# Performance work log

Hardware: AMD Instinct MI355X
Metric: run time of the kernel (lower is better)

## Reference

```python
import jax, jax.numpy as jnp
import numpy as np

B, S, DM, H, HD = 2, 2048, 1024, 16, 64
MEM_SIZE = 1000
K_SIMILAR, K_CONTIG = 8, 2
K_TOTAL = K_SIMILAR + K_CONTIG  # 10 memory tokens
NEG = -1e9


def setup_inputs() -> dict:
    key = jax.random.key(0)
    k1, k2, k3, k4, k5, k6 = jax.random.split(key, 6)
    inputs = jax.random.normal(k1, (B, S, DM), dtype=jnp.float32)
    attention_mask = jnp.ones((B, S), dtype=jnp.float32)
    Wq = jax.random.normal(k2, (DM, H * HD), dtype=jnp.float32) * 0.02
    Wk = jax.random.normal(k3, (DM, H * HD), dtype=jnp.float32) * 0.02
    Wv = jax.random.normal(k4, (DM, H * HD), dtype=jnp.float32) * 0.02
    Wo = jax.random.normal(k5, (H * HD, DM), dtype=jnp.float32) * 0.02
    events = jax.random.normal(k6, (MEM_SIZE, H * HD), dtype=jnp.float32) * 0.02
    return {"inputs": inputs, "attention_mask": attention_mask,
            "Wq": Wq, "Wk": Wk, "Wv": Wv, "Wo": Wo, "events": events}


def _forward(inputs, attention_mask, Wq, Wk, Wv, Wo, events):
    # projections (no bias), split heads: [B, H, S, HD]
    q = (inputs @ Wq).reshape(B, S, H, HD).transpose(0, 2, 1, 3)
    k = (inputs @ Wk).reshape(B, S, H, HD).transpose(0, 2, 1, 3)
    v = (inputs @ Wv).reshape(B, S, H, HD).transpose(0, 2, 1, 3)

    # --- episodic retrieval: cosine top-k of last-token key vs events ---
    qvec = k[:, :, -1, :].reshape(B, H * HD)                       # [B, D]
    qn = qvec / (jnp.linalg.norm(qvec, axis=-1, keepdims=True) + 1e-8)
    en = events / (jnp.linalg.norm(events, axis=-1, keepdims=True) + 1e-8)
    sims = qn @ en.T                                               # [B, M]
    _, topk_idx = jax.lax.top_k(sims, K_TOTAL)                     # [B, K]
    retrieved = events[topk_idx]                                   # [B, K, D]
    retrieved_k = retrieved.reshape(B, K_TOTAL, H, HD).transpose(0, 2, 1, 3)  # [B,H,K,HD]
    retrieved_v = retrieved_k                                      # non-differential path

    aug_k = jnp.concatenate([retrieved_k, k], axis=2)              # [B,H,K+S,HD]
    aug_v = jnp.concatenate([retrieved_v, v], axis=2)

    # --- ALiBi bias: slopes * (pos_i - pos_j) on original cols, 0 on memory cols ---
    slopes = 2.0 ** (-8.0 * jnp.arange(1, H + 1, dtype=jnp.float32) / H)  # [H]
    positions = jnp.arange(S, dtype=jnp.float32)
    pos_diff = positions[:, None] - positions[None, :]             # [S, S]
    alibi = slopes[:, None, None] * pos_diff                       # [H, S, S]
    alibi = jnp.concatenate([jnp.zeros((H, S, K_TOTAL), jnp.float32), alibi], axis=-1)

    # --- causal mask: -1e9 strictly-upper on original cols, 0 on memory cols ---
    tri = jnp.where(jnp.arange(S)[None, :] > jnp.arange(S)[:, None], NEG, 0.0)  # [S,S]
    causal = jnp.concatenate([jnp.zeros((S, K_TOTAL), jnp.float32), tri], axis=-1)

    # --- padding mask: memory tokens always attendable ---
    aug_mask = jnp.concatenate([jnp.ones((B, K_TOTAL), jnp.float32), attention_mask], axis=-1)
    mask_bias = (1.0 - aug_mask)[:, None, None, :] * NEG           # [B,1,1,K+S]

    scores = jnp.einsum("bhqd,bhkd->bhqk", q, aug_k) / np.sqrt(HD)
    scores = scores + alibi[None] + causal[None, None] + mask_bias
    attn = jax.nn.softmax(scores, axis=-1)
    out = jnp.einsum("bhqk,bhkd->bhqd", attn, aug_v)               # [B,H,S,HD]
    out = out.transpose(0, 2, 1, 3).reshape(B, S, H * HD)
    return out @ Wo


def reference(inputs, attention_mask, Wq, Wk, Wv, Wo, events):
    return _forward(inputs, attention_mask, Wq, Wk, Wv, Wo, events)
```

## Files before the change

kernel.cpp:

```cpp
#include <hip/hip_runtime.h>
#include <hip/hip_bf16.h>
#include <math.h>

#define B_   2
#define S_   2048
#define DM_  1024
#define H_   16
#define HD_  64
#define MEM_ 1000
#define KTOT 10
#define NROW (B_ * S_)
#define NEG9 (-1e9f)
#define LDK  72

#define NUNITS  1440
#define NSPLITI 416
#define PSLOT   4224
#define SC_  0.18033688f
#define TH_  170.238f

typedef __attribute__((ext_vector_type(8))) short short8;
typedef __attribute__((ext_vector_type(4))) float f32x4;

__device__ __forceinline__ float __exp2(float x) { return __builtin_amdgcn_exp2f(x); }

__device__ __forceinline__ void gll16(const __hip_bfloat16* g, __hip_bfloat16* l) {
    __builtin_amdgcn_global_load_lds(
        (const __attribute__((address_space(1))) void*)g,
        (__attribute__((address_space(3))) void*)l, 16, 0, 0);
}

__global__ __launch_bounds__(256) void prep(const float* __restrict__ inputs,
                                            const float* __restrict__ Wq,
                                            const float* __restrict__ Wk,
                                            const float* __restrict__ Wv,
                                            const float* __restrict__ Wo,
                                            __hip_bfloat16* __restrict__ Ax,
                                            __hip_bfloat16* __restrict__ Wt,
                                            float* __restrict__ lk,
                                            int* __restrict__ ctr) {
    const int bx = blockIdx.x, tid = threadIdx.x;
    if (bx == 0 && tid == 0) *ctr = 0;

    if (bx < 2048) {
        const size_t i = ((size_t)bx * 256 + tid) * 8;
        float4 a = *(const float4*)&inputs[i];
        float4 b = *(const float4*)&inputs[i + 4];
        alignas(16) __hip_bfloat16 t[8];
        t[0] = __float2bfloat16(a.x); t[1] = __float2bfloat16(a.y);
        t[2] = __float2bfloat16(a.z); t[3] = __float2bfloat16(a.w);
        t[4] = __float2bfloat16(b.x); t[5] = __float2bfloat16(b.y);
        t[6] = __float2bfloat16(b.z); t[7] = __float2bfloat16(b.w);
        *(short8*)&Ax[i] = *(short8*)t;
        return;
    }
    if (bx < 3072) {
        const int idx = bx - 2048;
        const int g = idx >> 8, rem = idx & 255;
        const float* W = (g == 0) ? Wq : (g == 1) ? Wk : (g == 2) ? Wv : Wo;
        const int n0 = (rem & 15) * 64, k0 = (rem >> 4) * 64;
        __shared__ float T[64][65];
        {
            const int r = tid >> 4, c4 = (tid & 15) * 4;
#pragma unroll
            for (int p = 0; p < 4; ++p) {
                float4 v = *(const float4*)&W[(size_t)(k0 + r + p * 16) * 1024 + n0 + c4];
                T[r + p * 16][c4 + 0] = v.x; T[r + p * 16][c4 + 1] = v.y;
                T[r + p * 16][c4 + 2] = v.z; T[r + p * 16][c4 + 3] = v.w;
            }
        }
        __syncthreads();
        {
            const int n = tid >> 3, off = (tid & 7) * 8;
#pragma unroll
            for (int p = 0; p < 2; ++p) {
                const int nn = n + p * 32;
                alignas(16) __hip_bfloat16 t[8];
#pragma unroll
                for (int j = 0; j < 8; ++j) t[j] = __float2bfloat16(T[off + j][nn]);
                *(short8*)&Wt[((size_t)(g * 1024 + n0 + nn)) * 1024 + k0 + off] = *(short8*)t;
            }
        }
        return;
    }
    {
        const int idx = bx - 3072;
        const int xblk = idx & 15, b = idx >> 4;
        const int cl = tid & 63;
        const int col = xblk * 64 + cl;
        const int kq = tid >> 6;
        __shared__ float xr[1024];
        __shared__ float part[4][64];
        for (int i = tid; i < 1024; i += 256)
            xr[i] = inputs[((size_t)(b * S_ + S_ - 1)) * 1024 + i];
        __syncthreads();
        float acc = 0.f;
#pragma unroll 4
        for (int k = kq * 256; k < kq * 256 + 256; ++k)
            acc += xr[k] * Wk[(size_t)k * 1024 + col];
        part[kq][cl] = acc;
        __syncthreads();
        if (tid < 64)
            lk[b * 1024 + xblk * 64 + tid] =
                part[0][tid] + part[1][tid] + part[2][tid] + part[3][tid];
    }
}

__device__ __forceinline__ void store_out(__hip_bfloat16* p, float x) { *p = __float2bfloat16(x); }
__device__ __forceinline__ void store_out(float* p, float x) { *p = x; }

template <typename OutT>
__global__ __launch_bounds__(256) void gemm_mfma(const __hip_bfloat16* __restrict__ A,
                                                 const __hip_bfloat16* __restrict__ Bt,
                                                 OutT* __restrict__ C, int ldc) {
    __shared__ __hip_bfloat16 As[128 * 32];
    __shared__ __hip_bfloat16 Bs[128 * 32];
    const int tid = threadIdx.x;
    const int wave = tid >> 6, lane = tid & 63;
    const int quad = lane >> 4, lm = lane & 15;
    const int wr = wave >> 1, wc = wave & 1;
    const int m0 = blockIdx.y * 128, n0 = blockIdx.x * 128;

    const int r0 = tid >> 2, c0 = (tid & 3) * 8;
    const __hip_bfloat16* ga0 = &A[(size_t)(m0 + r0) * 1024 + c0];
    const __hip_bfloat16* ga1 = &A[(size_t)(m0 + 64 + r0) * 1024 + c0];
    const __hip_bfloat16* gb0 = &Bt[(size_t)(n0 + r0) * 1024 + c0];
    const __hip_bfloat16* gb1 = &Bt[(size_t)(n0 + 64 + r0) * 1024 + c0];
    __hip_bfloat16* la0 = &As[(wave * 64) * 8];
    __hip_bfloat16* la1 = &As[(256 + wave * 64) * 8];
    __hip_bfloat16* lb0 = &Bs[(wave * 64) * 8];
    __hip_bfloat16* lb1 = &Bs[(256 + wave * 64) * 8];

    f32x4 acc[4][4];
#pragma unroll
    for (int i = 0; i < 4; ++i)
#pragma unroll
        for (int j = 0; j < 4; ++j) acc[i][j] = (f32x4){0.f, 0.f, 0.f, 0.f};

    for (int k0 = 0; k0 < 1024; k0 += 32) {
        __syncthreads();
        gll16(ga0 + k0, la0);
        gll16(ga1 + k0, la1);
        gll16(gb0 + k0, lb0);
        gll16(gb1 + k0, lb1);
        __syncthreads();
        short8 af[4], bf4[4];
#pragma unroll
        for (int mt = 0; mt < 4; ++mt)
            af[mt] = *(const short8*)&As[(wr * 64 + mt * 16 + lm) * 32 + quad * 8];
#pragma unroll
        for (int nt = 0; nt < 4; ++nt)
            bf4[nt] = *(const short8*)&Bs[(wc * 64 + nt * 16 + lm) * 32 + quad * 8];
#pragma unroll
        for (int mt = 0; mt < 4; ++mt)
#pragma unroll
            for (int nt = 0; nt < 4; ++nt)
                acc[mt][nt] = __builtin_amdgcn_mfma_f32_16x16x32_bf16(
                    af[mt], bf4[nt], acc[mt][nt], 0, 0, 0);
    }
#pragma unroll
    for (int mt = 0; mt < 4; ++mt)
#pragma unroll
        for (int nt = 0; nt < 4; ++nt) {
            const int col = n0 + wc * 64 + nt * 16 + lm;
#pragma unroll
            for (int i = 0; i < 4; ++i) {
                const int row = m0 + wr * 64 + mt * 16 + quad * 4 + i;
                store_out(&C[(size_t)row * ldc + col], acc[mt][nt][i]);
            }
        }
}

template <typename OutT>
__global__ __launch_bounds__(256) void gemm_mfma64(const __hip_bfloat16* __restrict__ A,
                                                   const __hip_bfloat16* __restrict__ Bt,
                                                   OutT* __restrict__ C, int ldc) {
    __shared__ __hip_bfloat16 As[64 * 32];
    __shared__ __hip_bfloat16 Bs[128 * 32];
    const int tid = threadIdx.x;
    const int wave = tid >> 6, lane = tid & 63;
    const int quad = lane >> 4, lm = lane & 15;
    const int wr = wave >> 1, wc = wave & 1;
    const int m0 = blockIdx.y * 64, n0 = blockIdx.x * 128;

    const int r0 = tid >> 2, c0 = (tid & 3) * 8;
    const __hip_bfloat16* ga  = &A[(size_t)(m0 + r0) * 1024 + c0];
    const __hip_bfloat16* gb0 = &Bt[(size_t)(n0 + r0) * 1024 + c0];
    const __hip_bfloat16* gb1 = &Bt[(size_t)(n0 + 64 + r0) * 1024 + c0];
    __hip_bfloat16* la  = &As[(wave * 64) * 8];
    __hip_bfloat16* lb0 = &Bs[(wave * 64) * 8];
    __hip_bfloat16* lb1 = &Bs[(256 + wave * 64) * 8];

    f32x4 acc[2][4];
#pragma unroll
    for (int i = 0; i < 2; ++i)
#pragma unroll
        for (int j = 0; j < 4; ++j) acc[i][j] = (f32x4){0.f, 0.f, 0.f, 0.f};

    for (int k0 = 0; k0 < 1024; k0 += 32) {
        __syncthreads();
        gll16(ga + k0, la);
        gll16(gb0 + k0, lb0);
        gll16(gb1 + k0, lb1);
        __syncthreads();
        short8 af[2], bf4[4];
#pragma unroll
        for (int mt = 0; mt < 2; ++mt)
            af[mt] = *(const short8*)&As[(wr * 32 + mt * 16 + lm) * 32 + quad * 8];
#pragma unroll
        for (int nt = 0; nt < 4; ++nt)
            bf4[nt] = *(const short8*)&Bs[(wc * 64 + nt * 16 + lm) * 32 + quad * 8];
#pragma unroll
        for (int mt = 0; mt < 2; ++mt)
#pragma unroll
            for (int nt = 0; nt < 4; ++nt)
                acc[mt][nt] = __builtin_amdgcn_mfma_f32_16x16x32_bf16(
                    af[mt], bf4[nt], acc[mt][nt], 0, 0, 0);
    }
#pragma unroll
    for (int mt = 0; mt < 2; ++mt)
#pragma unroll
        for (int nt = 0; nt < 4; ++nt) {
            const int col = n0 + wc * 64 + nt * 16 + lm;
#pragma unroll
            for (int i = 0; i < 4; ++i) {
                const int row = m0 + wr * 32 + mt * 16 + quad * 4 + i;
                store_out(&C[(size_t)row * ldc + col], acc[mt][nt][i]);
            }
        }
}

__global__ __launch_bounds__(256) void sims_kernel(const float* __restrict__ lk,
                                                   const float* __restrict__ events,
                                                   float* __restrict__ sims) {
    const int b = blockIdx.y;
    const int tid = threadIdx.x;
    const int wave = tid >> 6, lane = tid & 63;
    __shared__ float qv[1024];
    for (int i = tid; i < 1024; i += 256)
        qv[i] = lk[b * 1024 + i];
    __syncthreads();

    const int m = blockIdx.x * 4 + wave;
    if (m >= MEM_) return;
    const float* ev = &events[(size_t)m * 1024];
    float dot = 0.f, nrm = 0.f;
    for (int d = lane; d < 1024; d += 64) {
        float e = ev[d];
        dot += qv[d] * e;
        nrm += e * e;
    }
    for (int off = 32; off; off >>= 1) {
        dot += __shfl_down(dot, off);
        nrm += __shfl_down(nrm, off);
    }
    if (lane == 0) sims[b * 1024 + m] = dot / (sqrtf(nrm) + 1e-8f);
}

__global__ __launch_bounds__(64) void topk10_kernel(const float* __restrict__ sims,
                                                    int* __restrict__ topk) {
    const int b = blockIdx.x;
    const int lane = threadIdx.x;
    const int base = lane * 16;
    float v[16];
#pragma unroll
    for (int j = 0; j < 16; ++j) {
        const int m = base + j;
        v[j] = (m < MEM_) ? sims[b * 1024 + m] : -INFINITY;
    }
    for (int it = 0; it < KTOT; ++it) {
        float best = -INFINITY; int bi = 0x7fffffff;
#pragma unroll
        for (int j = 0; j < 16; ++j)
            if (v[j] > best) { best = v[j]; bi = base + j; }
        for (int off = 32; off; off >>= 1) {
            const float ob = __shfl_xor(best, off);
            const int   oi = __shfl_xor(bi, off);
            if (ob > best || (ob == best && oi < bi)) { best = ob; bi = oi; }
        }
        if (lane == 0) topk[b * KTOT + it] = bi;
#pragma unroll
        for (int j = 0; j < 16; ++j)
            if (base + j == bi) v[j] = -INFINITY;
    }
}

__global__ __launch_bounds__(256) void attn_mfma(
        const __hip_bfloat16* __restrict__ qkv,
        const float* __restrict__ events,
        const int* __restrict__ topk,
        const float* __restrict__ amask,
        __hip_bfloat16* __restrict__ out,
        int* __restrict__ ctr,
        float* __restrict__ partb) {
    const int tid = threadIdx.x;
    const int wave = tid >> 6, lane = tid & 63;
    const int quad = lane >> 4, lm = lane & 15;

    const __hip_bfloat16* qf = qkv;
    const __hip_bfloat16* kf = qkv + 1024;
    const __hip_bfloat16* vf = qkv + 2048;

    __shared__ __hip_bfloat16 Ks[64 * LDK];
    __shared__ __hip_bfloat16 Vt[80 * LDK];
    __shared__ __hip_bfloat16 Ps[64 * LDK];
    __shared__ float colb[64];
    __shared__ float redb[4];
    __shared__ int sItem;

    const int va = tid & 31, vdc = tid >> 5;
    const int vtok0 = va * 2, vd0 = vdc * 8;

    for (int i = tid * 8; i < 64 * LDK; i += 256 * 8)
        *(int4*)&Vt[i] = make_int4(0, 0, 0, 0);
    for (int i = tid; i < 16 * LDK; i += 256) {
        const int r = i / LDK;
        Vt[64 * LDK + i] = __float2bfloat16(r == 0 ? 1.0f : 0.0f);
    }

    for (;;) {
        __syncthreads();
        if (tid == 0) sItem = atomicAdd(ctr, 1);
        __syncthreads();
        const int n = sItem;
        if (n >= NUNITS) break;

        int qt, inner, kstart, kend, prt = 0, sidx = 0;
        bool haveMem, split;
        {
            int sel;
            if (n < 96)        { qt = 18 - (n >> 5); inner = n & 31; sel = 2; }
            else if (n < 160)  { const int m = n - 96; inner = m & 31;
                                 if (m < 32) { qt = 31; sel = 0; } else { qt = 15; sel = 2; } }
            else if (n < 288)  { const int m = n - 160; const int s4 = m >> 5; inner = m & 31;
                                 if (s4 == 0)      { qt = 31; sel = 1; }
                                 else if (s4 == 1) { qt = 30; sel = 0; }
                                 else if (s4 == 2) { qt = 30; sel = 1; }
                                 else              { qt = 14; sel = 2; } }
            else if (n < 1344) { const int m = n - 288; const int g = m / 96, r = m - g * 96;
                                 sel = r >> 5; inner = r & 31;
                                 qt = (sel < 2) ? (29 - g) : (13 - g); }
            else               { const int m = n - 1344; qt = 2 - (m >> 5); inner = m & 31; sel = 2; }
            if (sel == 2) { kstart = 0; kend = qt; haveMem = true; split = false; }
            else {
                const int mid = (qt + 1) >> 1;
                prt = sel;
                kstart = prt ? mid : 0;
                kend   = prt ? qt : (mid - 1);
                haveMem = (prt == 0);
                split = true;
                sidx = (31 - qt) * 32 + inner;
            }
        }
        const int q0 = qt * 64;
        const int h = 15 - ((inner >> 1) & 15);
        const int b = inner & 1;
        const float slope2 = __exp2(-0.5f * (float)(h + 1)) * 1.44269504f;

        short8 pk[2], pv0, pv1;
        float pam = 1.f;
        auto prefetchKV = [&](int kt) {
            const __hip_bfloat16* ks = &kf[((size_t)(b * S_ + kt * 64)) * 3072 + h * 64];
#pragma unroll
            for (int u = 0; u < 2; ++u) {
                int c = tid * 2 + u, row = c >> 3, off = (c & 7) * 8;
                pk[u] = *(const short8*)&ks[(size_t)row * 3072 + off];
            }
            const __hip_bfloat16* v0 =
                &vf[((size_t)(b * S_ + kt * 64 + vtok0)) * 3072 + h * 64 + vd0];
            pv0 = *(const short8*)v0;
            pv1 = *(const short8*)(v0 + 3072);
            if (tid < 64) pam = amask[b * S_ + kt * 64 + tid];
        };
        auto stageKV = [&](int kt) {
#pragma unroll
            for (int u = 0; u < 2; ++u) {
                int c = tid * 2 + u, row = c >> 3, off = (c & 7) * 8;
                *(short8*)&Ks[row * LDK + off] = pk[u];
            }
#pragma unroll
            for (int j = 0; j < 8; ++j) {
                short2 pr; pr.x = pv0[j]; pr.y = pv1[j];
                *(short2*)&Vt[(vd0 + j) * LDK + vtok0] = pr;
            }
            if (tid < 64)
                colb[tid] = fmaf(-slope2, (float)(kt * 64 + tid), (1.f - pam) * NEG9);
        };

        prefetchKV(kstart);

        short8 qa[2];
        {
            const __hip_bfloat16* qsrc =
                &qf[((size_t)(b * S_ + q0 + wave * 16 + lm)) * 3072 + h * 64 + quad * 8];
            qa[0] = *(const short8*)qsrc;
            qa[1] = *(const short8*)(qsrc + 32);
        }
        if (haveMem && tid < 80) {
            const int tok = tid >> 3, d0 = (tid & 7) * 8;
            const int ev = topk[b * KTOT + tok];
            const float* es = &events[(size_t)ev * 1024 + h * 64 + d0];
#pragma unroll
            for (int j = 0; j < 8; ++j) {
                __hip_bfloat16 x = __float2bfloat16(es[j]);
                Ks[tok * LDK + d0 + j] = x;
                Vt[(d0 + j) * LDK + tok] = x;
            }
        }

        float m_[4], mshift[4];
        f32x4 Oa[5];
#pragma unroll
        for (int i = 0; i < 4; ++i) {
            m_[i] = -INFINITY;
            mshift[i] = -slope2 * (float)(q0 + wave * 16 + quad * 4 + i);
        }
#pragma unroll
        for (int nt = 0; nt < 5; ++nt) Oa[nt] = (f32x4){0.f, 0.f, 0.f, 0.f};

        auto qk = [&](f32x4* sa) {
#pragma unroll
            for (int nt = 0; nt < 4; ++nt) sa[nt] = (f32x4){0.f, 0.f, 0.f, 0.f};
#pragma unroll
            for (int ks2 = 0; ks2 < 2; ++ks2) {
#pragma unroll
                for (int nt = 0; nt < 4; ++nt) {
                    short8 bk = *(const short8*)&Ks[(nt * 16 + lm) * LDK + ks2 * 32 + quad * 8];
                    sa[nt] = __builtin_amdgcn_mfma_f32_16x16x32_bf16(qa[ks2], bk, sa[nt], 0, 0, 0);
                }
            }
        };
        auto pv = [&]() {
#pragma unroll
            for (int ks2 = 0; ks2 < 2; ++ks2) {
                short8 ap = *(const short8*)&Ps[(wave * 16 + lm) * LDK + ks2 * 32 + quad * 8];
#pragma unroll
                for (int nt = 0; nt < 5; ++nt) {
                    short8 bv = *(const short8*)&Vt[(nt * 16 + lm) * LDK + ks2 * 32 + quad * 8];
                    Oa[nt] = __builtin_amdgcn_mfma_f32_16x16x32_bf16(ap, bv, Oa[nt], 0, 0, 0);
                }
            }
        };

        auto softmax_online = [&](const f32x4* sa, int kt, bool diag) {
            float cb[4];
            if (kt >= 0) {
#pragma unroll
                for (int nt = 0; nt < 4; ++nt) cb[nt] = colb[nt * 16 + lm];
            }
#pragma unroll
            for (int i = 0; i < 4; ++i) {
                const int lr = wave * 16 + quad * 4 + i;
                const int rg = q0 + lr;
                float s[4];
#pragma unroll
                for (int nt = 0; nt < 4; ++nt) {
                    const int cc = nt * 16 + lm;
                    if (kt < 0) {
                        s[nt] = (cc < KTOT) ? fmaf(sa[nt][i], SC_, mshift[i]) : NEG9;
                    } else {
                        float v = fmaf(sa[nt][i], SC_, cb[nt]);
                        s[nt] = (diag && kt * 64 + cc > rg) ? NEG9 : v;
                    }
                }
                float rmax = fmaxf(fmaxf(s[0], s[1]), fmaxf(s[2], s[3]));
#pragma unroll
                for (int off = 1; off < 16; off <<= 1)
                    rmax = fmaxf(rmax, __shfl_xor(rmax, off, 16));
                const float newm = fmaxf(m_[i], rmax);
                const float al = __exp2(m_[i] - newm);
                m_[i] = newm;
#pragma unroll
                for (int nt = 0; nt < 4; ++nt)
                    Ps[lr * LDK + nt * 16 + lm] = __float2bfloat16(__exp2(s[nt] - newm));
#pragma unroll
                for (int nt = 0; nt < 5; ++nt)
                    Oa[nt][i] *= al;
            }
        };

        auto softmax_fast = [&](const f32x4* sa, int cbase, bool diag) {
            float cb[4];
#pragma unroll
            for (int nt = 0; nt < 4; ++nt) cb[nt] = colb[nt * 16 + lm];
#pragma unroll
            for (int i = 0; i < 4; ++i) {
                const int lr = wave * 16 + quad * 4 + i;
                const float cm = m_[i];
                float p[4];
#pragma unroll
                for (int nt = 0; nt < 4; ++nt)
                    p[nt] = __exp2(fmaf(sa[nt][i], SC_, cb[nt]) - cm);
                if (diag) {
                    const int rg = q0 + lr;
#pragma unroll
                    for (int nt = 0; nt < 4; ++nt)
                        if (cbase + nt * 16 + lm > rg) p[nt] = 0.f;
                }
#pragma unroll
                for (int nt = 0; nt < 4; ++nt)
                    Ps[lr * LDK + nt * 16 + lm] = __float2bfloat16(p[nt]);
            }
        };

        if (haveMem) {
            __syncthreads();
            f32x4 sa[4];
            qk(sa);
            softmax_online(sa, -1, false);
            pv();
            __syncthreads();
        }
        stageKV(kstart);
        if (kstart < kend) prefetchKV(kstart + 1);
        __syncthreads();
        {
            f32x4 sa[4];
            qk(sa);
            softmax_online(sa, kstart, kstart == qt);
            pv();
        }

        int kend2 = kstart;
        if (kend > kstart) {
            float mloc = fminf(fminf(m_[0], m_[1]), fminf(m_[2], m_[3]));
#pragma unroll
            for (int off = 1; off < 64; off <<= 1)
                mloc = fminf(mloc, __shfl_xor(mloc, off, 64));
            if (lane == 0) redb[wave] = mloc;
            __syncthreads();
            const float mmin = fminf(fminf(redb[0], redb[1]), fminf(redb[2], redb[3]));
            kend2 = min(kend, (int)((TH_ - mmin) / (64.f * slope2)));
        }
        for (int kt = kstart + 1; kt <= kend2; ++kt) {
            __syncthreads();
            stageKV(kt);
            if (kt < kend2) prefetchKV(kt + 1);
            __syncthreads();
            f32x4 sa[4];
            qk(sa);
            softmax_fast(sa, kt * 64, kt == qt);
            pv();
        }

        float l_[4];
#pragma unroll
        for (int i = 0; i < 4; ++i) l_[i] = __shfl(Oa[4][i], (lane & 48));
        if (!split) {
#pragma unroll
            for (int i = 0; i < 4; ++i) {
                const int lr = wave * 16 + quad * 4 + i;
                const float inv = 1.f / l_[i];
                __hip_bfloat16* dst = &out[((size_t)(b * S_ + q0 + lr)) * 1024 + h * 64 + lm];
#pragma unroll
                for (int nt = 0; nt < 4; ++nt)
                    dst[nt * 16] = __float2bfloat16(Oa[nt][i] * inv);
            }
        } else {
            float* psl = partb + (size_t)(sidx * 2 + prt) * PSLOT;
#pragma unroll
            for (int i = 0; i < 4; ++i) {
                const int lr = wave * 16 + quad * 4 + i;
#pragma unroll
                for (int nt = 0; nt < 4; ++nt)
                    psl[lr * 64 + nt * 16 + lm] = Oa[nt][i];
                if (lm == 0) {
                    psl[4096 + lr] = m_[i];
                    psl[4160 + lr] = l_[i];
                }
            }
        }
    }
}

__global__ __launch_bounds__(256) void merge_split(const float* __restrict__ partb,
                                                   __hip_bfloat16* __restrict__ out) {
    const int sidx = blockIdx.x;
    const int qt = 31 - (sidx >> 5);
    const int inner = sidx & 31;
    const int h = 15 - ((inner >> 1) & 15);
    const int b = inner & 1;
    const int q0 = qt * 64;
    const float* pA = partb + (size_t)(sidx * 2) * PSLOT;
    const float* pB = pA + PSLOT;
    const int t = threadIdx.x;
    const int row = t >> 2, c0 = (t & 3) * 16;

    const float mA = pA[4096 + row], lA = pA[4160 + row];
    const float mB = pB[4096 + row], lB = pB[4160 + row];
    const float mm = fmaxf(mA, mB);
    const float fA = __exp2(mA - mm), fB = __exp2(mB - mm);
    const float inv = 1.f / (lA * fA + lB * fB);
    const float wA = fA * inv, wB = fB * inv;

    __hip_bfloat16* dst = &out[((size_t)(b * S_ + q0 + row)) * 1024 + h * 64 + c0];
    alignas(16) __hip_bfloat16 tmp[16];
#pragma unroll
    for (int j = 0; j < 16; j += 4) {
        f32x4 a = *(const f32x4*)&pA[row * 64 + c0 + j];
        f32x4 v = *(const f32x4*)&pB[row * 64 + c0 + j];
#pragma unroll
        for (int e = 0; e < 4; ++e)
            tmp[j + e] = __float2bfloat16(a[e] * wA + v[e] * wB);
    }
    *(short8*)&dst[0] = *(short8*)&tmp[0];
    *(short8*)&dst[8] = *(short8*)&tmp[8];
}

extern "C" void kernel_launch(void* const* d_in, const int* in_sizes, int n_in,
                              void* d_out, int out_size, void* d_ws, size_t ws_size,
                              hipStream_t stream) {
    const float* inputs = (const float*)d_in[0];
    const float* amask  = (const float*)d_in[1];
    const float* Wq     = (const float*)d_in[2];
    const float* Wk     = (const float*)d_in[3];
    const float* Wv     = (const float*)d_in[4];
    const float* Wo     = (const float*)d_in[5];
    const float* events = (const float*)d_in[6];
    float* out = (float*)d_out;

    __hip_bfloat16* Ax  = (__hip_bfloat16*)d_ws;
    __hip_bfloat16* Wt  = Ax + (size_t)NROW * 1024;
    __hip_bfloat16* qkv = Wt + (size_t)4096 * 1024;
    __hip_bfloat16* ao  = qkv + (size_t)NROW * 3072;
    float* lk   = (float*)(ao + (size_t)NROW * 1024);
    float* sims = lk + 2 * 1024;
    int* topk   = (int*)(sims + 2 * 1024);
    int* ctr    = topk + B_ * KTOT;
    float* partb = (float*)d_ws;

    dim3 blk(256);
    prep<<<3104, blk, 0, stream>>>(inputs, Wq, Wk, Wv, Wo, Ax, Wt, lk, ctr);
    sims_kernel<<<dim3(250, B_), blk, 0, stream>>>(lk, events, sims);
    topk10_kernel<<<B_, 64, 0, stream>>>(sims, topk);
    gemm_mfma<__hip_bfloat16><<<dim3(24, 32), blk, 0, stream>>>(Ax, Wt, qkv, 3072);
    attn_mfma<<<1024, blk, 0, stream>>>(qkv, events, topk, amask, ao, ctr, partb);
    merge_split<<<NSPLITI, blk, 0, stream>>>(partb, ao);
    gemm_mfma64<float><<<dim3(8, 64), blk, 0, stream>>>(
        ao, Wt + (size_t)3072 * 1024, out, 1024);
}
```

Measured before the change: 255.6 us.

## Partition attention work queue into eight per-XCD counters for L2 locality

Replaces the single global atomic work counter with eight counters keyed by blockIdx.x&7, so each group of blocks (likely one per XCD) processes only its own set of four (batch, head) slices. A table-driven order of 45 q-tile/part entries replaces the old arithmetic schedule, with each group walking the same descending-cost ordering. The aim is to keep the K/V data of a head inside one XCD's L2 and to reduce contention on the atomic counter. The trade-off is that load balancing becomes per-group, so one XCD may finish later than the others.

```diff
diff --git a/kernel.cpp b/kernel.cpp
--- a/kernel.cpp
+++ b/kernel.cpp
@@ -12,8 +12,7 @@
 #define NROW (B_ * S_)
 #define NEG9 (-1e9f)
 #define LDK  72
-
-#define NUNITS  1440
+#define QITEMS 180
 #define NSPLITI 416
 #define PSLOT   4224
 #define SC_  0.18033688f
@@ -29,6 +28,14 @@
         (const __attribute__((address_space(1))) void*)g,
         (__attribute__((address_space(3))) void*)l, 16, 0, 0);
 }
+
+__device__ const unsigned char UORD[45] = {
+    74, 70, 66, 124, 62, 125, 120, 121, 116, 58,
+    117, 112, 113, 108, 54, 109, 104, 105, 100, 50,
+    101, 96, 97, 92, 46, 93, 88, 89, 84, 42,
+    85, 80, 81, 76, 38, 77, 34, 30, 26, 22,
+    18, 14, 10, 6, 2
+};
 
 __global__ __launch_bounds__(256) void prep(const float* __restrict__ inputs,
                                             const float* __restrict__ Wq,
@@ -40,7 +47,7 @@
                                             float* __restrict__ lk,
                                             int* __restrict__ ctr) {
     const int bx = blockIdx.x, tid = threadIdx.x;
-    if (bx == 0 && tid == 0) *ctr = 0;
+    if (bx == 0 && tid < 8) ctr[tid] = 0;
 
     if (bx < 2048) {
         const size_t i = ((size_t)bx * 256 + tid) * 8;
@@ -296,6 +303,7 @@
     const int tid = threadIdx.x;
     const int wave = tid >> 6, lane = tid & 63;
     const int quad = lane >> 4, lm = lane & 15;
+    const int g = blockIdx.x & 7;
 
     const __hip_bfloat16* qf = qkv;
     const __hip_bfloat16* kf = qkv + 1024;
@@ -320,41 +328,23 @@
 
     for (;;) {
         __syncthreads();
-        if (tid == 0) sItem = atomicAdd(ctr, 1);
+        if (tid == 0) sItem = atomicAdd(&ctr[g], 1);
         __syncthreads();
         const int n = sItem;
-        if (n >= NUNITS) break;
-
-        int qt, inner, kstart, kend, prt = 0, sidx = 0;
-        bool haveMem, split;
-        {
-            int sel;
-            if (n < 96)        { qt = 18 - (n >> 5); inner = n & 31; sel = 2; }
-            else if (n < 160)  { const int m = n - 96; inner = m & 31;
-                                 if (m < 32) { qt = 31; sel = 0; } else { qt = 15; sel = 2; } }
-            else if (n < 288)  { const int m = n - 160; const int s4 = m >> 5; inner = m & 31;
-                                 if (s4 == 0)      { qt = 31; sel = 1; }
-                                 else if (s4 == 1) { qt = 30; sel = 0; }
-                                 else if (s4 == 2) { qt = 30; sel = 1; }
-                                 else              { qt = 14; sel = 2; } }
-            else if (n < 1344) { const int m = n - 288; const int g = m / 96, r = m - g * 96;
-                                 sel = r >> 5; inner = r & 31;
-                                 qt = (sel < 2) ? (29 - g) : (13 - g); }
-            else               { const int m = n - 1344; qt = 2 - (m >> 5); inner = m & 31; sel = 2; }
-            if (sel == 2) { kstart = 0; kend = qt; haveMem = true; split = false; }
-            else {
-                const int mid = (qt + 1) >> 1;
-                prt = sel;
-                kstart = prt ? mid : 0;
-                kend   = prt ? qt : (mid - 1);
-                haveMem = (prt == 0);
-                split = true;
-                sidx = (31 - qt) * 32 + inner;
-            }
-        }
+        if (n >= QITEMS) break;
+
+        const int entry = UORD[n >> 2];
+        const int qt = entry >> 2, part = entry & 3;
+        const int s = g * 4 + (n & 3);
+        const int h = 15 - (s >> 1);
+        const int b = s & 1;
+        const bool split = (part < 2);
+        const int mid = (qt + 1) >> 1;
+        const int kstart = (part == 1) ? mid : 0;
+        const int kend   = (part == 0) ? (mid - 1) : qt;
+        const bool haveMem = (part != 1);
+        const int sidx = (31 - qt) * 32 + s;
         const int q0 = qt * 64;
-        const int h = 15 - ((inner >> 1) & 15);
-        const int b = inner & 1;
         const float slope2 = __exp2(-0.5f * (float)(h + 1)) * 1.44269504f;
 
         short8 pk[2], pv0, pv1;
@@ -452,18 +442,18 @@
             for (int i = 0; i < 4; ++i) {
                 const int lr = wave * 16 + quad * 4 + i;
                 const int rg = q0 + lr;
-                float s[4];
+                float s2[4];
 #pragma unroll
                 for (int nt = 0; nt < 4; ++nt) {
                     const int cc = nt * 16 + lm;
                     if (kt < 0) {
-                        s[nt] = (cc < KTOT) ? fmaf(sa[nt][i], SC_, mshift[i]) : NEG9;
+                        s2[nt] = (cc < KTOT) ? fmaf(sa[nt][i], SC_, mshift[i]) : NEG9;
                     } else {
                         float v = fmaf(sa[nt][i], SC_, cb[nt]);
-                        s[nt] = (diag && kt * 64 + cc > rg) ? NEG9 : v;
+                        s2[nt] = (diag && kt * 64 + cc > rg) ? NEG9 : v;
                     }
                 }
-                float rmax = fmaxf(fmaxf(s[0], s[1]), fmaxf(s[2], s[3]));
+                float rmax = fmaxf(fmaxf(s2[0], s2[1]), fmaxf(s2[2], s2[3]));
 #pragma unroll
                 for (int off = 1; off < 16; off <<= 1)
                     rmax = fmaxf(rmax, __shfl_xor(rmax, off, 16));
@@ -472,7 +462,7 @@
                 m_[i] = newm;
 #pragma unroll
                 for (int nt = 0; nt < 4; ++nt)
-                    Ps[lr * LDK + nt * 16 + lm] = __float2bfloat16(__exp2(s[nt] - newm));
+                    Ps[lr * LDK + nt * 16 + lm] = __float2bfloat16(__exp2(s2[nt] - newm));
 #pragma unroll
                 for (int nt = 0; nt < 5; ++nt)
                     Oa[nt][i] *= al;
@@ -557,7 +547,7 @@
                     dst[nt * 16] = __float2bfloat16(Oa[nt][i] * inv);
             }
         } else {
-            float* psl = partb + (size_t)(sidx * 2 + prt) * PSLOT;
+            float* psl = partb + (size_t)(sidx * 2 + part) * PSLOT;
 #pragma unroll
             for (int i = 0; i < 4; ++i) {
                 const int lr = wave * 16 + quad * 4 + i;
@@ -577,9 +567,9 @@
                                                    __hip_bfloat16* __restrict__ out) {
     const int sidx = blockIdx.x;
     const int qt = 31 - (sidx >> 5);
-    const int inner = sidx & 31;
-    const int h = 15 - ((inner >> 1) & 15);
-    const int b = inner & 1;
+    const int s = sidx & 31;
+    const int h = 15 - (s >> 1);
+    const int b = s & 1;
     const int q0 = qt * 64;
     const float* pA = partb + (size_t)(sidx * 2) * PSLOT;
     const float* pB = pA + PSLOT;
```

Measured after the change: 259.6 us. Within noise of the previous version (+1.5%).
